# Kernel tuning notes

Hardware: AMD Instinct MI355X
Metric: run time of the kernel (lower is better)

## Reference

```python
import jax, jax.numpy as jnp
import numpy as np

# Static config (matches init_kwargs)
B, H, W, C = 8, 80, 60, 512
WS, SHIFT = 10, 5
NH = 16
HD = C // NH  # 32
L = WS * WS  # 100 tokens per window
NW = (H // WS) * (W // WS)  # 48 windows per image
EPS = 1e-5


def _relative_position_index():
    coords = np.stack(np.meshgrid(np.arange(WS), np.arange(WS), indexing='ij'))  # (2,WS,WS)
    flat = coords.reshape(2, -1)  # (2, L)
    rel = flat[:, :, None] - flat[:, None, :]  # (2, L, L)
    rel = rel.transpose(1, 2, 0)  # (L, L, 2)
    rel[:, :, 0] += WS - 1
    rel[:, :, 1] += WS - 1
    rel[:, :, 0] *= 2 * WS - 1
    return rel.sum(-1)  # (L, L) indices into (2*WS-1)^2 table


def _attn_mask():
    # Swin shift mask: label 3x3 regions, tokens in different regions cannot attend.
    img = np.zeros((H, W), dtype=np.float32)
    slices = (slice(0, -WS), slice(-WS, -SHIFT), slice(-SHIFT, None))
    cnt = 0
    for hs in slices:
        for ws_ in slices:
            img[hs, ws_] = cnt
            cnt += 1
    mw = img.reshape(H // WS, WS, W // WS, WS).transpose(0, 2, 1, 3).reshape(NW, L)
    diff = mw[:, None, :] - mw[:, :, None]  # (NW, L, L)
    return np.where(diff != 0, -100.0, 0.0).astype(np.float32)


REL_IDX = jnp.asarray(_relative_position_index())
ATTN_MASK = jnp.asarray(_attn_mask())


def layernorm(x, g, b):
    mu = jnp.mean(x, axis=-1, keepdims=True)
    var = jnp.mean(jnp.square(x - mu), axis=-1, keepdims=True)
    return (x - mu) * jax.lax.rsqrt(var + EPS) * g + b


def setup_inputs() -> dict:
    key = jax.random.key(0)
    ks = jax.random.split(key, 8)
    s = 0.02
    return {
        'hidden_states': jax.random.normal(ks[0], (B, H * W, C), jnp.float32),
        'ln1_g': jnp.ones((C,), jnp.float32),
        'ln1_b': jnp.zeros((C,), jnp.float32),
        'wq': jax.random.normal(ks[1], (C, C), jnp.float32) * s,
        'bq': jnp.zeros((C,), jnp.float32),
        'wk': jax.random.normal(ks[2], (C, C), jnp.float32) * s,
        'bk': jnp.zeros((C,), jnp.float32),
        'wv': jax.random.normal(ks[3], (C, C), jnp.float32) * s,
        'bv': jnp.zeros((C,), jnp.float32),
        'wo': jax.random.normal(ks[4], (C, C), jnp.float32) * s,
        'bo': jnp.zeros((C,), jnp.float32),
        'rel_bias_table': jax.random.normal(ks[5], ((2 * WS - 1) ** 2, NH), jnp.float32) * s,
        'ln2_g': jnp.ones((C,), jnp.float32),
        'ln2_b': jnp.zeros((C,), jnp.float32),
        'w1': jax.random.normal(ks[6], (C, 4 * C), jnp.float32) * s,
        'b1': jnp.zeros((4 * C,), jnp.float32),
        'w2': jax.random.normal(ks[7], (4 * C, C), jnp.float32) * s,
        'b2': jnp.zeros((C,), jnp.float32),
    }


def reference(hidden_states, ln1_g, ln1_b, wq, bq, wk, bk, wv, bv, wo, bo,
              rel_bias_table, ln2_g, ln2_b, w1, b1, w2, b2):
    shortcut = hidden_states  # (B, H*W, C)
    x = layernorm(hidden_states, ln1_g, ln1_b).reshape(B, H, W, C)
    # cyclic shift (H, W divisible by WS -> no padding needed)
    x = jnp.roll(x, (-SHIFT, -SHIFT), axis=(1, 2))
    # window partition -> (B*NW, L, C)
    win = x.reshape(B, H // WS, WS, W // WS, WS, C).transpose(0, 1, 3, 2, 4, 5)
    win = win.reshape(B * NW, L, C)
    # multi-head attention within windows
    q = (win @ wq + bq).reshape(-1, L, NH, HD).transpose(0, 2, 1, 3)
    k = (win @ wk + bk).reshape(-1, L, NH, HD).transpose(0, 2, 1, 3)
    v = (win @ wv + bv).reshape(-1, L, NH, HD).transpose(0, 2, 1, 3)
    scores = jnp.einsum('bhqd,bhkd->bhqk', q, k) / np.sqrt(HD).astype(np.float32)
    bias = rel_bias_table[REL_IDX.reshape(-1)].reshape(L, L, NH).transpose(2, 0, 1)
    scores = scores + bias[None]  # (B*NW, NH, L, L)
    scores = scores.reshape(B, NW, NH, L, L) + ATTN_MASK[None, :, None]
    attn = jax.nn.softmax(scores.reshape(B * NW, NH, L, L), axis=-1)
    ctx = jnp.einsum('bhqk,bhkd->bhqd', attn, v).transpose(0, 2, 1, 3).reshape(B * NW, L, C)
    out = ctx @ wo + bo
    # window reverse + un-shift
    out = out.reshape(B, H // WS, W // WS, WS, WS, C).transpose(0, 1, 3, 2, 4, 5)
    out = out.reshape(B, H, W, C)
    out = jnp.roll(out, (SHIFT, SHIFT), axis=(1, 2)).reshape(B, H * W, C)
    hs = shortcut + out
    # FFN with post-residual layernorm input
    y = layernorm(hs, ln2_g, ln2_b)
    y = jax.nn.gelu(y @ w1 + b1, approximate=False) @ w2 + b2
    return hs + y
```

## Files before the change

### kernel.cpp

```cpp
#include <hip/hip_runtime.h>
#include <math.h>

typedef unsigned short u16;
typedef unsigned int u32;
typedef __bf16 bf16x8 __attribute__((ext_vector_type(8)));
typedef float f32x4 __attribute__((ext_vector_type(4)));

__device__ __forceinline__ float b2f(u16 u) { return __uint_as_float(((u32)u) << 16); }
__device__ __forceinline__ u16 f2b(float f) {
    u32 x = __float_as_uint(f);
    return (u16)((x + 0x7FFFu + ((x >> 16) & 1u)) >> 16);
}
__device__ __forceinline__ void load8f(const float* p, size_t idx, float* o) {
    const float4* q = (const float4*)(p + idx);
    float4 a = q[0], b = q[1];
    o[0]=a.x; o[1]=a.y; o[2]=a.z; o[3]=a.w; o[4]=b.x; o[5]=b.y; o[6]=b.z; o[7]=b.w;
}
__device__ __forceinline__ void gld16(const void* g, void* l) {
    __builtin_amdgcn_global_load_lds(
        (const __attribute__((address_space(1))) u32*)g,
        (__attribute__((address_space(3))) u32*)l, 16, 0, 0);
}

__global__ __launch_bounds__(256) void transpose_k(const float* __restrict__ Win, u16* __restrict__ Wt,
                                                   int Kd, int Nd, float scale) {
    __shared__ u16 tile[32][33];
    int tx = threadIdx.x & 31, ty = threadIdx.x >> 5;
    int k0 = blockIdx.x << 5, n0 = blockIdx.y << 5;
#pragma unroll
    for (int r = 0; r < 4; r++)
        tile[ty + 8 * r][tx] = f2b(Win[(size_t)(k0 + ty + 8 * r) * Nd + (n0 + tx)] * scale);
    __syncthreads();
#pragma unroll
    for (int r = 0; r < 4; r++)
        Wt[(size_t)(n0 + ty + 8 * r) * Kd + (k0 + tx)] = tile[tx][ty + 8 * r];
}

__global__ __launch_bounds__(256) void ln1win_k(const float* __restrict__ x, const float* __restrict__ g,
                                                const float* __restrict__ bta, u16* __restrict__ win) {
    int wave = threadIdx.x >> 6, lane = threadIdx.x & 63;
    int token = blockIdx.x * 4 + wave;
    int b = token / 4800, rem = token - b * 4800;
    int h = rem / 60, w = rem - h * 60;
    int hr = h + 75; if (hr >= 80) hr -= 80;
    int wr = w + 55; if (wr >= 60) wr -= 60;
    int widx = (hr / 10) * 6 + (wr / 10);
    int l = (hr - (hr / 10) * 10) * 10 + (wr - (wr / 10) * 10);
    size_t dstrow = ((size_t)b * 48 + widx) * 100 + l;
    int c0 = lane * 8;
    float v[8]; load8f(x, (size_t)token * 512 + c0, v);
    float s = 0.f, s2 = 0.f;
#pragma unroll
    for (int e = 0; e < 8; e++) { s += v[e]; s2 += v[e] * v[e]; }
#pragma unroll
    for (int o = 32; o > 0; o >>= 1) { s += __shfl_xor(s, o); s2 += __shfl_xor(s2, o); }
    float mean = s * (1.0f / 512.0f);
    float var = fmaxf(s2 * (1.0f / 512.0f) - mean * mean, 0.0f);
    float rstd = rsqrtf(var + 1e-5f);
    uint4 o4; u16* ou = (u16*)&o4;
#pragma unroll
    for (int e = 0; e < 8; e++)
        ou[e] = f2b((v[e] - mean) * rstd * g[c0 + e] + bta[c0 + e]);
    *(uint4*)(win + dstrow * 512 + c0) = o4;
}

__global__ __launch_bounds__(256) void resid2_k(const float* __restrict__ shortcut, const u16* __restrict__ attn_out,
                                                const float* __restrict__ g, const float* __restrict__ bta,
                                                u16* __restrict__ hs, u16* __restrict__ ln2y) {
    int wave = threadIdx.x >> 6, lane = threadIdx.x & 63;
    int token = blockIdx.x * 4 + wave;
    int b = token / 4800, rem = token - b * 4800;
    int h = rem / 60, w = rem - h * 60;
    int hr = h + 75; if (hr >= 80) hr -= 80;
    int wr = w + 55; if (wr >= 60) wr -= 60;
    int widx = (hr / 10) * 6 + (wr / 10);
    int l = (hr - (hr / 10) * 10) * 10 + (wr - (wr / 10) * 10);
    size_t arow = ((size_t)b * 48 + widx) * 100 + l;
    int c0 = lane * 8;
    float sv[8]; load8f(shortcut, (size_t)token * 512 + c0, sv);
    uint4 da = *(const uint4*)(attn_out + arow * 512 + c0);
    const u16* au = (const u16*)&da;
    float hv[8]; float s = 0.f, s2 = 0.f;
    uint4 oh; u16* ohu = (u16*)&oh;
#pragma unroll
    for (int e = 0; e < 8; e++) {
        hv[e] = sv[e] + b2f(au[e]);
        s += hv[e]; s2 += hv[e] * hv[e];
        ohu[e] = f2b(hv[e]);
    }
    *(uint4*)(hs + (size_t)token * 512 + c0) = oh;
#pragma unroll
    for (int off = 32; off > 0; off >>= 1) { s += __shfl_xor(s, off); s2 += __shfl_xor(s2, off); }
    float mean = s * (1.0f / 512.0f);
    float var = fmaxf(s2 * (1.0f / 512.0f) - mean * mean, 0.0f);
    float rstd = rsqrtf(var + 1e-5f);
    uint4 oy; u16* oyu = (u16*)&oy;
#pragma unroll
    for (int e = 0; e < 8; e++)
        oyu[e] = f2b((hv[e] - mean) * rstd * g[c0 + e] + bta[c0 + e]);
    *(uint4*)(ln2y + (size_t)token * 512 + c0) = oy;
}

template <int EPI, int OF32>
__global__ __launch_bounds__(256) void gemm_k(const u16* __restrict__ A, const u16* __restrict__ Bt,
                                              const float* __restrict__ bias, const u16* __restrict__ res,
                                              void* __restrict__ C, float bscale, int M, int N, int K) {
    __shared__ __align__(16) u16 As[128 * 32];
    __shared__ __align__(16) u16 Bs[128 * 32];
    int tid = threadIdx.x;
    int wave = tid >> 6, lane = tid & 63;
    int l15 = lane & 15, quad = lane >> 4;
    int lq = lane >> 2, lr = lane & 3;
    int wm = (wave >> 1) * 64, wn = (wave & 1) * 64;
    int bm = blockIdx.x, bn = blockIdx.y;

    f32x4 acc[4][4];
#pragma unroll
    for (int i = 0; i < 4; i++)
#pragma unroll
        for (int j = 0; j < 4; j++) acc[i][j] = (f32x4){0.f, 0.f, 0.f, 0.f};

    const u16* Ab = A + (size_t)(bm * 128) * K;
    const u16* Bb = Bt + (size_t)(bn * 128) * K;

    for (int kt = 0; kt < K; kt += 32) {
#pragma unroll
        for (int h = 0; h < 2; h++) {
            int r = h * 64 + wave * 16 + lq;
            gld16(Ab + (size_t)r * K + kt + lr * 8, &As[(h * 64 + wave * 16) * 32]);
            gld16(Bb + (size_t)r * K + kt + lr * 8, &Bs[(h * 64 + wave * 16) * 32]);
        }
        __syncthreads();
        bf16x8 af[4], bfr[4];
#pragma unroll
        for (int t = 0; t < 4; t++) {
            af[t]  = *(const bf16x8*)(&As[(wm + t * 16 + l15) * 32 + quad * 8]);
            bfr[t] = *(const bf16x8*)(&Bs[(wn + t * 16 + l15) * 32 + quad * 8]);
        }
#pragma unroll
        for (int i = 0; i < 4; i++)
#pragma unroll
            for (int j = 0; j < 4; j++)
                acc[i][j] = __builtin_amdgcn_mfma_f32_16x16x32_bf16(af[i], bfr[j], acc[i][j], 0, 0, 0);
        __syncthreads();
    }

#pragma unroll
    for (int i = 0; i < 4; i++) {
        int row0 = bm * 128 + wm + i * 16 + quad * 4;
#pragma unroll
        for (int j = 0; j < 4; j++) {
            int col = bn * 128 + wn + j * 16 + l15;
            float bv = bias[col] * bscale;
#pragma unroll
            for (int rr = 0; rr < 4; rr++) {
                int row = row0 + rr;
                float v = acc[i][j][rr] + bv;
                if (EPI == 1) {
                    float zz = 1.5957691216f * (v + 0.044715f * v * v * v);
                    float t = 1.0f - 2.0f / (__expf(zz) + 1.0f);
                    v = 0.5f * v * (1.0f + t);
                }
                if (EPI == 2) v += b2f(res[(size_t)row * 512 + col]);
                if (OF32) ((float*)C)[(size_t)row * N + col] = v;
                else      ((u16*)C)[(size_t)row * N + col] = f2b(v);
            }
        }
    }
}

__global__ __launch_bounds__(256) void biasprep_k(const float* __restrict__ table, u16* __restrict__ biasM) {
    int idx = blockIdx.x * 256 + threadIdx.x;
    int k = idx % 112;
    int t = idx / 112;
    int q = t % 100; t /= 100;
    int head = t & 15, wt = t >> 4;
    float v;
    if (k >= 100) {
        v = -1e30f;
    } else {
        int qi = q / 10, qj = q - qi * 10;
        int ki = k / 10, kj = k - ki * 10;
        int rel = (qi - ki) * 19 + (qj - kj) + 180;
        v = table[rel * 16 + head];
        int rq = ((wt & 2) ? (qi < 5 ? 4 : 8) : 0) + ((wt & 1) ? (qj < 5 ? 1 : 2) : 0);
        int rk = ((wt & 2) ? (ki < 5 ? 4 : 8) : 0) + ((wt & 1) ? (kj < 5 ? 1 : 2) : 0);
        if (rq != rk) v -= 100.0f;
    }
    biasM[idx] = f2b(v);
}

__global__ __launch_bounds__(256, 3) void attn_mfma_k(const u16* __restrict__ Q, const u16* __restrict__ Km,
                                                      const u16* __restrict__ V, const u16* __restrict__ biasM,
                                                      u16* __restrict__ ctx) {
    __shared__ __align__(16) u16 lds[4 * 6144];
    int tid = threadIdx.x;
    int wave = tid >> 6, lane = tid & 63;
    int l15 = lane & 15, quad = lane >> 4;
    int bid = blockIdx.x;
    int win = bid >> 2;
    int head = ((bid & 3) << 2) + wave;
    int w48 = win % 48;
    int wh = w48 / 6, ww = w48 - wh * 6;
    int wtype = ((wh == 7) ? 2 : 0) + ((ww == 5) ? 1 : 0);
    size_t base = (size_t)win * 51200 + head * 32;
    u16* Vt = lds + wave * 6144;
    u16* Pl = Vt + 4096;
    const u16* bptr = biasM + (size_t)(wtype * 16 + head) * 11200;

    {
        uint4 z = {0u, 0u, 0u, 0u};
#pragma unroll
        for (int r = 0; r < 2; r++) {
            int c = r * 64 + lane;
            int d = c >> 2, seg = c & 3;
            int k0 = 96 + seg * 8;
            *(uint4*)(Vt + d * 128 + (k0 ^ ((d & 7) << 3))) = z;
        }
        uint2 z2 = {0u, 0u};
        *(uint2*)(Pl + l15 * 128 + ((112 + quad * 4) ^ ((l15 & 7) << 3))) = z2;
    }
#pragma unroll
    for (int r = 0; r < 2; r++) {
        int k = r * 64 + lane;
        if (k < 100) {
            const uint4* vp = (const uint4*)(V + base + (size_t)k * 512);
#pragma unroll
            for (int c = 0; c < 4; c++) {
                uint4 dv = vp[c];
                const u16* e = (const u16*)&dv;
#pragma unroll
                for (int t = 0; t < 8; t++) {
                    int d = c * 8 + t;
                    Vt[d * 128 + (k ^ ((d & 7) << 3))] = e[t];
                }
            }
        }
    }
    bf16x8 kf[7];
#pragma unroll
    for (int i = 0; i < 7; i++) {
        int kr = i * 16 + l15; if (kr > 99) kr = 99;
        kf[i] = *(const bf16x8*)(Km + base + (size_t)kr * 512 + quad * 8);
    }
    bf16x8 vf[2][4];
#pragma unroll
    for (int it = 0; it < 2; it++)
#pragma unroll
        for (int ks = 0; ks < 4; ks++) {
            int D = it * 16 + l15;
            vf[it][ks] = *(const bf16x8*)(Vt + D * 128 + ((ks * 32 + quad * 8) ^ ((D & 7) << 3)));
        }

#pragma unroll 1
    for (int j = 0; j < 7; j++) {
        int q = j * 16 + l15;
        int qc = q > 99 ? 99 : q;
        bf16x8 qf = *(const bf16x8*)(Q + base + (size_t)qc * 512 + quad * 8);
        f32x4 s[7];
#pragma unroll
        for (int i = 0; i < 7; i++) {
            uint2 bb = *(const uint2*)(bptr + (size_t)qc * 112 + i * 16 + quad * 4);
            const u16* be = (const u16*)&bb;
            s[i][0] = b2f(be[0]); s[i][1] = b2f(be[1]);
            s[i][2] = b2f(be[2]); s[i][3] = b2f(be[3]);
        }
#pragma unroll
        for (int i = 0; i < 7; i++)
            s[i] = __builtin_amdgcn_mfma_f32_16x16x32_bf16(kf[i], qf, s[i], 0, 0, 0);
        float m = -1e30f;
#pragma unroll
        for (int i = 0; i < 7; i++)
#pragma unroll
            for (int rr = 0; rr < 4; rr++) m = fmaxf(m, s[i][rr]);
        m = fmaxf(m, __shfl_xor(m, 16));
        m = fmaxf(m, __shfl_xor(m, 32));
        float l = 0.f;
#pragma unroll
        for (int i = 0; i < 7; i++)
#pragma unroll
            for (int rr = 0; rr < 4; rr++) { s[i][rr] = __expf(s[i][rr] - m); l += s[i][rr]; }
        l += __shfl_xor(l, 16);
        l += __shfl_xor(l, 32);
#pragma unroll
        for (int i = 0; i < 7; i++) {
            u32 lo, hi;
            asm("v_cvt_pk_bf16_f32 %0, %1, %2" : "=v"(lo) : "v"(s[i][0]), "v"(s[i][1]));
            asm("v_cvt_pk_bf16_f32 %0, %1, %2" : "=v"(hi) : "v"(s[i][2]), "v"(s[i][3]));
            uint2 w; w.x = lo; w.y = hi;
            *(uint2*)(Pl + l15 * 128 + ((i * 16 + quad * 4) ^ ((l15 & 7) << 3))) = w;
        }
        f32x4 o0 = (f32x4){0.f, 0.f, 0.f, 0.f};
        f32x4 o1 = (f32x4){0.f, 0.f, 0.f, 0.f};
#pragma unroll
        for (int ks = 0; ks < 4; ks++) {
            bf16x8 pf = *(const bf16x8*)(Pl + l15 * 128 + ((ks * 32 + quad * 8) ^ ((l15 & 7) << 3)));
            o0 = __builtin_amdgcn_mfma_f32_16x16x32_bf16(vf[0][ks], pf, o0, 0, 0, 0);
            o1 = __builtin_amdgcn_mfma_f32_16x16x32_bf16(vf[1][ks], pf, o1, 0, 0, 0);
        }
        float inv = 1.0f / l;
        if (q < 100) {
            u16* cp = ctx + base + (size_t)q * 512;
            {
                float a0 = o0[0]*inv, a1 = o0[1]*inv, a2 = o0[2]*inv, a3 = o0[3]*inv;
                u32 lo, hi;
                asm("v_cvt_pk_bf16_f32 %0, %1, %2" : "=v"(lo) : "v"(a0), "v"(a1));
                asm("v_cvt_pk_bf16_f32 %0, %1, %2" : "=v"(hi) : "v"(a2), "v"(a3));
                uint2 w; w.x = lo; w.y = hi;
                *(uint2*)(cp + quad * 4) = w;
            }
            {
                float a0 = o1[0]*inv, a1 = o1[1]*inv, a2 = o1[2]*inv, a3 = o1[3]*inv;
                u32 lo, hi;
                asm("v_cvt_pk_bf16_f32 %0, %1, %2" : "=v"(lo) : "v"(a0), "v"(a1));
                asm("v_cvt_pk_bf16_f32 %0, %1, %2" : "=v"(hi) : "v"(a2), "v"(a3));
                uint2 w; w.x = lo; w.y = hi;
                *(uint2*)(cp + 16 + quad * 4) = w;
            }
        }
    }
}

extern "C" void kernel_launch(void* const* d_in, const int* in_sizes, int n_in,
                              void* d_out, int out_size, void* d_ws, size_t ws_size,
                              hipStream_t stream) {
    const float* hidden = (const float*)d_in[0];
    const float* ln1_g  = (const float*)d_in[1];
    const float* ln1_b  = (const float*)d_in[2];
    const float* wq = (const float*)d_in[3];  const float* bq = (const float*)d_in[4];
    const float* wk = (const float*)d_in[5];  const float* bk = (const float*)d_in[6];
    const float* wv = (const float*)d_in[7];  const float* bv = (const float*)d_in[8];
    const float* wo = (const float*)d_in[9];  const float* bo = (const float*)d_in[10];
    const float* rel = (const float*)d_in[11];
    const float* ln2_g = (const float*)d_in[12];
    const float* ln2_b = (const float*)d_in[13];
    const float* w1 = (const float*)d_in[14]; const float* b1 = (const float*)d_in[15];
    const float* w2 = (const float*)d_in[16]; const float* b2 = (const float*)d_in[17];

    const size_t NTC = 38400ull * 512;
    u16* ws = (u16*)d_ws;
    u16* R0 = ws;
    u16* R1 = ws + NTC;
    u16* Rh = ws + 2 * NTC;
    u16* wqt = ws + 3 * NTC;
    u16* wkt = wqt + 512 * 512;
    u16* wvt = wkt + 512 * 512;
    u16* wot = wvt + 512 * 512;
    u16* w1t = wot + 512 * 512;
    u16* w2t = w1t + 1048576;
    u16* dlo = (u16*)d_out;
    u16* biasM = dlo + NTC;
    float* outp = (float*)d_out;

    const float SC = 0.17677669529663689f;

    transpose_k<<<dim3(16, 16), 256, 0, stream>>>(wq, wqt, 512, 512, SC);
    transpose_k<<<dim3(16, 16), 256, 0, stream>>>(wk, wkt, 512, 512, 1.0f);
    transpose_k<<<dim3(16, 16), 256, 0, stream>>>(wv, wvt, 512, 512, 1.0f);
    transpose_k<<<dim3(16, 16), 256, 0, stream>>>(wo, wot, 512, 512, 1.0f);
    transpose_k<<<dim3(16, 64), 256, 0, stream>>>(w1, w1t, 512, 2048, 1.0f);
    transpose_k<<<dim3(64, 16), 256, 0, stream>>>(w2, w2t, 2048, 512, 1.0f);

    biasprep_k<<<2800, 256, 0, stream>>>(rel, biasM);

    ln1win_k<<<9600, 256, 0, stream>>>(hidden, ln1_g, ln1_b, R0 );

    gemm_k<0, 0><<<dim3(300, 4), 256, 0, stream>>>(R0, wqt, bq, nullptr, R1 , SC, 38400, 512, 512);
    gemm_k<0, 0><<<dim3(300, 4), 256, 0, stream>>>(R0, wkt, bk, nullptr, Rh , 1.0f, 38400, 512, 512);
    gemm_k<0, 0><<<dim3(300, 4), 256, 0, stream>>>(R0, wvt, bv, nullptr, dlo , 1.0f, 38400, 512, 512);

    attn_mfma_k<<<1536, 256, 0, stream>>>(R1, Rh, dlo, biasM, R0 );

    gemm_k<0, 0><<<dim3(300, 4), 256, 0, stream>>>(R0, wot, bo, nullptr, R1 , 1.0f, 38400, 512, 512);

    resid2_k<<<9600, 256, 0, stream>>>(hidden, R1, ln2_g, ln2_b, Rh , dlo );

    for (int mc = 3; mc >= 0; mc--) {
        size_t roff = (size_t)mc * 9600 * 512;
        gemm_k<1, 0><<<dim3(75, 16), 256, 0, stream>>>(dlo + roff, w1t, b1, nullptr, R0 ,
                                                       1.0f, 9600, 2048, 512);
        gemm_k<2, 1><<<dim3(75, 4), 256, 0, stream>>>(R0, w2t, b2, Rh + roff, outp + roff,
                                                      1.0f, 9600, 512, 2048);
    }
}
```

Baseline: 806.7 us.

## Fuse QKV GEMMs, triple-buffer GEMM k-loop, remap blocks across XCDs, halve FFN chunks

The three Q/K/V projections are fused into one GEMM launch, since wq, wk and wv are stored contiguously and the concatenated bias is built by a new small kernel. The output is routed to separate buffers by column block. The GEMM k-loop becomes a three-stage LDS pipeline using async global-to-LDS loads with explicit vmcnt waits, replacing the synchronous load-then-compute loop. Workgroup IDs are remapped so that consecutive tiles land on the same XCD for L2 locality. The FFN now runs in two larger chunks instead of four. Together these aim to cut launch overhead and memory stalls, at the cost of three times more LDS per block, which may lower occupancy.

```diff
diff --git a/kernel.cpp b/kernel.cpp
--- a/kernel.cpp
+++ b/kernel.cpp
@@ -34,6 +34,13 @@
 #pragma unroll
     for (int r = 0; r < 4; r++)
         Wt[(size_t)(n0 + ty + 8 * r) * Kd + (k0 + tx)] = tile[tx][ty + 8 * r];
+}
+
+__global__ __launch_bounds__(256) void biascat_k(const float* __restrict__ bq, const float* __restrict__ bk,
+                                                 const float* __restrict__ bv, float* __restrict__ o) {
+    int i = blockIdx.x * 256 + threadIdx.x;
+    float v = (i < 512) ? bq[i] * 0.17677669529663689f : (i < 1024 ? bk[i - 512] : bv[i - 1024]);
+    o[i] = v;
 }
 
 __global__ __launch_bounds__(256) void ln1win_k(const float* __restrict__ x, const float* __restrict__ g,
@@ -101,18 +108,26 @@
     *(uint4*)(ln2y + (size_t)token * 512 + c0) = oy;
 }
 
-template <int EPI, int OF32>
+template <int EPI, int OF32, int QKV>
 __global__ __launch_bounds__(256) void gemm_k(const u16* __restrict__ A, const u16* __restrict__ Bt,
                                               const float* __restrict__ bias, const u16* __restrict__ res,
-                                              void* __restrict__ C, float bscale, int M, int N, int K) {
-    __shared__ __align__(16) u16 As[128 * 32];
-    __shared__ __align__(16) u16 Bs[128 * 32];
+                                              void* __restrict__ C0, void* __restrict__ C1, void* __restrict__ C2,
+                                              int M, int N, int K) {
+    __shared__ __align__(16) u16 As[3][128 * 32];
+    __shared__ __align__(16) u16 Bs[3][128 * 32];
     int tid = threadIdx.x;
     int wave = tid >> 6, lane = tid & 63;
     int l15 = lane & 15, quad = lane >> 4;
     int lq = lane >> 2, lr = lane & 3;
     int wm = (wave >> 1) * 64, wn = (wave & 1) * 64;
-    int bm = blockIdx.x, bn = blockIdx.y;
+
+    int gx = gridDim.x, gy = gridDim.y;
+    int nwg = gx * gy;
+    int orig = blockIdx.x * gy + blockIdx.y;
+    int q8 = nwg >> 3, r8 = nwg & 7;
+    int xcd = orig & 7, loc = orig >> 3;
+    int wg = (xcd < r8 ? xcd * (q8 + 1) : r8 * (q8 + 1) + (xcd - r8) * q8) + loc;
+    int bn = wg % gy, bm = wg / gy;
 
     f32x4 acc[4][4];
 #pragma unroll
@@ -123,35 +138,57 @@
     const u16* Ab = A + (size_t)(bm * 128) * K;
     const u16* Bb = Bt + (size_t)(bn * 128) * K;
 
-    for (int kt = 0; kt < K; kt += 32) {
+    int T = K >> 5;
+    auto STAGE = [&](int b, int t) {
+        int kt = t << 5;
 #pragma unroll
         for (int h = 0; h < 2; h++) {
             int r = h * 64 + wave * 16 + lq;
-            gld16(Ab + (size_t)r * K + kt + lr * 8, &As[(h * 64 + wave * 16) * 32]);
-            gld16(Bb + (size_t)r * K + kt + lr * 8, &Bs[(h * 64 + wave * 16) * 32]);
-        }
-        __syncthreads();
+            gld16(Ab + (size_t)r * K + kt + lr * 8, &As[b][(h * 64 + wave * 16) * 32]);
+            gld16(Bb + (size_t)r * K + kt + lr * 8, &Bs[b][(h * 64 + wave * 16) * 32]);
+        }
+    };
+
+    STAGE(0, 0);
+    STAGE(1, 1);
+    for (int t = 0; t < T; t++) {
+        int cb = t % 3;
+        if (t + 2 < T) STAGE((t + 2) % 3, t + 2);
+        if (t + 2 < T)      asm volatile("s_waitcnt vmcnt(8)" ::: "memory");
+        else if (t + 1 < T) asm volatile("s_waitcnt vmcnt(4)" ::: "memory");
+        else                asm volatile("s_waitcnt vmcnt(0)" ::: "memory");
+        __builtin_amdgcn_s_barrier();
+        asm volatile("" ::: "memory");
         bf16x8 af[4], bfr[4];
 #pragma unroll
-        for (int t = 0; t < 4; t++) {
-            af[t]  = *(const bf16x8*)(&As[(wm + t * 16 + l15) * 32 + quad * 8]);
-            bfr[t] = *(const bf16x8*)(&Bs[(wn + t * 16 + l15) * 32 + quad * 8]);
-        }
+        for (int x = 0; x < 4; x++) {
+            af[x]  = *(const bf16x8*)(&As[cb][(wm + x * 16 + l15) * 32 + quad * 8]);
+            bfr[x] = *(const bf16x8*)(&Bs[cb][(wn + x * 16 + l15) * 32 + quad * 8]);
+        }
+        asm volatile("s_waitcnt lgkmcnt(0)" ::: "memory");
+        __builtin_amdgcn_sched_barrier(0);
+        __builtin_amdgcn_s_barrier();
+        asm volatile("" ::: "memory");
 #pragma unroll
         for (int i = 0; i < 4; i++)
 #pragma unroll
             for (int j = 0; j < 4; j++)
                 acc[i][j] = __builtin_amdgcn_mfma_f32_16x16x32_bf16(af[i], bfr[j], acc[i][j], 0, 0, 0);
-        __syncthreads();
-    }
-
+    }
+
+    u16* Cd = (u16*)C0;
+    if (QKV) {
+        int sel = bn >> 2;
+        Cd = (sel == 0) ? (u16*)C0 : (sel == 1) ? (u16*)C1 : (u16*)C2;
+    }
 #pragma unroll
     for (int i = 0; i < 4; i++) {
         int row0 = bm * 128 + wm + i * 16 + quad * 4;
 #pragma unroll
         for (int j = 0; j < 4; j++) {
-            int col = bn * 128 + wn + j * 16 + l15;
-            float bv = bias[col] * bscale;
+            int colg = bn * 128 + wn + j * 16 + l15;
+            int col = QKV ? (colg & 511) : colg;
+            float bv = bias[colg];
 #pragma unroll
             for (int rr = 0; rr < 4; rr++) {
                 int row = row0 + rr;
@@ -162,8 +199,8 @@
                     v = 0.5f * v * (1.0f + t);
                 }
                 if (EPI == 2) v += b2f(res[(size_t)row * 512 + col]);
-                if (OF32) ((float*)C)[(size_t)row * N + col] = v;
-                else      ((u16*)C)[(size_t)row * N + col] = f2b(v);
+                if (OF32) ((float*)Cd)[(size_t)row * N + col] = v;
+                else      ((u16*)Cd)[(size_t)row * N + col] = f2b(v);
             }
         }
     }
@@ -348,6 +385,7 @@
     u16* wot = wvt + 512 * 512;
     u16* w1t = wot + 512 * 512;
     u16* w2t = w1t + 1048576;
+    float* qkvb = (float*)(w2t + 1048576);
     u16* dlo = (u16*)d_out;
     u16* biasM = dlo + NTC;
     float* outp = (float*)d_out;
@@ -360,26 +398,26 @@
     transpose_k<<<dim3(16, 16), 256, 0, stream>>>(wo, wot, 512, 512, 1.0f);
     transpose_k<<<dim3(16, 64), 256, 0, stream>>>(w1, w1t, 512, 2048, 1.0f);
     transpose_k<<<dim3(64, 16), 256, 0, stream>>>(w2, w2t, 2048, 512, 1.0f);
-
+    biascat_k<<<6, 256, 0, stream>>>(bq, bk, bv, qkvb);
     biasprep_k<<<2800, 256, 0, stream>>>(rel, biasM);
 
     ln1win_k<<<9600, 256, 0, stream>>>(hidden, ln1_g, ln1_b, R0 );
 
-    gemm_k<0, 0><<<dim3(300, 4), 256, 0, stream>>>(R0, wqt, bq, nullptr, R1 , SC, 38400, 512, 512);
-    gemm_k<0, 0><<<dim3(300, 4), 256, 0, stream>>>(R0, wkt, bk, nullptr, Rh , 1.0f, 38400, 512, 512);
-    gemm_k<0, 0><<<dim3(300, 4), 256, 0, stream>>>(R0, wvt, bv, nullptr, dlo , 1.0f, 38400, 512, 512);
+    gemm_k<0, 0, 1><<<dim3(300, 12), 256, 0, stream>>>(R0, wqt, qkvb, nullptr,
+                                                       R1 , Rh , dlo , 38400, 512, 512);
 
     attn_mfma_k<<<1536, 256, 0, stream>>>(R1, Rh, dlo, biasM, R0 );
 
-    gemm_k<0, 0><<<dim3(300, 4), 256, 0, stream>>>(R0, wot, bo, nullptr, R1 , 1.0f, 38400, 512, 512);
+    gemm_k<0, 0, 0><<<dim3(300, 4), 256, 0, stream>>>(R0, wot, bo, nullptr,
+                                                      R1 , nullptr, nullptr, 38400, 512, 512);
 
     resid2_k<<<9600, 256, 0, stream>>>(hidden, R1, ln2_g, ln2_b, Rh , dlo );
 
-    for (int mc = 3; mc >= 0; mc--) {
-        size_t roff = (size_t)mc * 9600 * 512;
-        gemm_k<1, 0><<<dim3(75, 16), 256, 0, stream>>>(dlo + roff, w1t, b1, nullptr, R0 ,
-                                                       1.0f, 9600, 2048, 512);
-        gemm_k<2, 1><<<dim3(75, 4), 256, 0, stream>>>(R0, w2t, b2, Rh + roff, outp + roff,
-                                                      1.0f, 9600, 512, 2048);
-    }
-}
+    for (int mc = 1; mc >= 0; mc--) {
+        size_t roff = (size_t)mc * 19200 * 512;
+        gemm_k<1, 0, 0><<<dim3(150, 16), 256, 0, stream>>>(dlo + roff, w1t, b1, nullptr,
+                                                           R0 , nullptr, nullptr, 19200, 2048, 512);
+        gemm_k<2, 1, 0><<<dim3(150, 4), 256, 0, stream>>>(R0, w2t, b2, Rh + roff,
+                                                          outp + roff, nullptr, nullptr, 19200, 512, 2048);
+    }
+}
```

Result: faster. 749.8 us (-7.1%).
